# Kernel optimization log

Hardware: AMD Instinct MI355X
Metric: run time of the kernel (lower is better)

The kernel has to match this reference:

```python
import jax, jax.numpy as jnp
import numpy as np
import math
from jax import lax

DIM = 128
D_STATE = 16
D_CONV = 4
EXPAND = 2
NSLICES = 16
D_INNER = EXPAND * DIM          # 256
DT_RANK = math.ceil(DIM / 16)   # 8
B_, H_, W_ = 4, 64, 64
L = H_ * W_                     # 4096


def silu(x):
    return x * jax.nn.sigmoid(x)


def causal_conv1d(x, w, b):
    # x: (b, d, l), w: (d, k) depthwise, b: (d,)  -- causal, output length l
    l = x.shape[-1]
    xp = jnp.pad(x, ((0, 0), (0, 0), (D_CONV - 1, 0)))
    y = sum(w[None, :, k, None] * xp[:, :, k:k + l] for k in range(D_CONV))
    return y + b[None, :, None]


def selective_scan(u, delta, A, B, C):
    # u, delta: (b, d, l); A: (d, n); B, C: (b, n, l)
    bsz, d, l = u.shape
    n = A.shape[1]
    u_t = u.transpose(2, 0, 1)      # (l, b, d)
    d_t = delta.transpose(2, 0, 1)  # (l, b, d)
    B_t = B.transpose(2, 0, 1)      # (l, b, n)
    C_t = C.transpose(2, 0, 1)      # (l, b, n)

    def step(h, inp):
        u_, de_, b_, c_ = inp
        dA = jnp.exp(de_[..., None] * A)                    # (b, d, n)
        h = h * dA + (de_ * u_)[..., None] * b_[:, None, :]  # (b, d, n)
        y = jnp.einsum('bdn,bn->bd', h, c_)
        return h, y

    h0 = jnp.zeros((bsz, d, n), u.dtype)
    _, ys = lax.scan(step, h0, (u_t, d_t, B_t, C_t))
    return ys.transpose(1, 2, 0)  # (b, d, l)


def mamba_dir(xz, conv_w, conv_b, x_proj_w, dt_w, dt_b, A_log, Dp):
    # one directional Mamba branch (conv + S6 scan + silu(z) gating), returns (b, d_inner, l)
    x, z = jnp.split(xz, 2, axis=1)
    x = silu(causal_conv1d(x, conv_w, conv_b))
    x_dbl = jnp.einsum('rd,bdl->brl', x_proj_w, x)          # (b, dt_rank+2n, l)
    dt_raw = x_dbl[:, :DT_RANK]
    Bm = x_dbl[:, DT_RANK:DT_RANK + D_STATE]
    Cm = x_dbl[:, DT_RANK + D_STATE:]
    delta = jax.nn.softplus(jnp.einsum('dr,brl->bdl', dt_w, dt_raw) + dt_b[None, :, None])
    A = -jnp.exp(A_log)
    y = selective_scan(x, delta, A, Bm, Cm)
    y = y + Dp[None, :, None] * x
    return y * silu(z)


def setup_inputs() -> dict:
    key = jax.random.key(0)
    ks = iter(jax.random.split(key, 40))

    def rn(shape, scale=0.02):
        return jax.random.normal(next(ks), shape, dtype=jnp.float32) * scale

    inp = {"x_in": jax.random.normal(next(ks), (B_, H_, W_, DIM), dtype=jnp.float32)}
    inp["in_proj_w"] = rn((2 * D_INNER, DIM))
    for suf in ["", "_b", "_s"]:
        inp["conv_w" + suf] = rn((D_INNER, D_CONV), 0.1)
        inp["conv_b" + suf] = rn((D_INNER,), 0.1)
        inp["x_proj_w" + suf] = rn((DT_RANK + 2 * D_STATE, D_INNER))
        inp["dt_proj_w" + suf] = rn((D_INNER, DT_RANK), 0.1)
        inp["dt_proj_b" + suf] = rn((D_INNER,), 0.1)
        inp["A_log" + suf] = jnp.log(jnp.tile(jnp.arange(1, D_STATE + 1, dtype=jnp.float32), (D_INNER, 1)))
        inp["D" + suf] = jnp.ones((D_INNER,), jnp.float32)
    inp["out_proj_w"] = rn((DIM, D_INNER))
    return inp


def reference(x_in, in_proj_w, conv_w, conv_b, x_proj_w, dt_proj_w, dt_proj_b, A_log, D,
              conv_w_b, conv_b_b, x_proj_w_b, dt_proj_w_b, dt_proj_b_b, A_log_b, D_b,
              conv_w_s, conv_b_s, x_proj_w_s, dt_proj_w_s, dt_proj_b_s, A_log_s, D_s,
              out_proj_w):
    b, h, w, c = x_in.shape
    l = h * w
    x = x_in.reshape(b, l, c)
    xz = jnp.einsum('pd,bld->bpl', in_proj_w, x)  # (b, 2*d_inner, l)

    # forward scan
    y_f = mamba_dir(xz, conv_w, conv_b, x_proj_w, dt_proj_w, dt_proj_b, A_log, D)
    # backward scan (flip along length)
    y_b = jnp.flip(mamba_dir(jnp.flip(xz, -1), conv_w_b, conv_b_b, x_proj_w_b,
                             dt_proj_w_b, dt_proj_b_b, A_log_b, D_b), -1)
    # interleaved-slice scan: chunk length into NSLICES pieces, stack, flatten
    m = l // NSLICES
    xz_s = xz.reshape(b, 2 * D_INNER, NSLICES, m).swapaxes(-1, -2).reshape(b, 2 * D_INNER, l)
    y_s = mamba_dir(xz_s, conv_w_s, conv_b_s, x_proj_w_s, dt_proj_w_s, dt_proj_b_s, A_log_s, D_s)
    y_s = y_s.reshape(b, D_INNER, m, NSLICES).swapaxes(-1, -2).reshape(b, D_INNER, l)

    y = y_f + y_b + y_s
    out = jnp.einsum('od,bdl->blo', out_proj_w, y)
    return out.reshape(b, h, w, c)
```

## Files before the change

### kernel.cpp

```cpp
#include <hip/hip_runtime.h>
#include <math.h>

#define LSEQ 4096

#define XZ_OFF   0ULL
#define XZ_SZ    (4ULL * 4096 * 512)
#define U_OFF    (XZ_OFF + XZ_SZ)
#define DIR_SZ   (4ULL * 256 * 4096)
#define DELTA_OFF (U_OFF + 3ULL * DIR_SZ)
#define BC_OFF   (DELTA_OFF + 3ULL * DIR_SZ)
#define BC_SZ    (4ULL * 4096 * 32)
#define WTIN_OFF DELTA_OFF
#define WTOUT_OFF U_OFF

__device__ __forceinline__ float sigmoidf_(float x) { return 1.0f / (1.0f + __expf(-x)); }
__device__ __forceinline__ float siluf_(float x)    { return x * sigmoidf_(x); }

__device__ __forceinline__ float fast_exp2_asm(float x) {
    float r;
    asm volatile("v_exp_f32 %0, %1\n\ts_nop 0" : "=v"(r) : "v"(x));
    return r;
}
#if defined(__has_builtin)
#if __has_builtin(__builtin_amdgcn_exp2f)
#define EXP2(x) __builtin_amdgcn_exp2f(x)
#else
#define EXP2(x) fast_exp2_asm(x)
#endif
#else
#define EXP2(x) fast_exp2_asm(x)
#endif

__device__ __forceinline__ float softplus_fast(float x) {
    float t = EXP2(1.44269504f * x);
    float r = 0.69314718f * __log2f(1.0f + t);
    return (x > 20.0f) ? x : r;
}

__device__ __forceinline__ int perm_idx(int dir, int j) {
    if (dir == 0) return j;
    if (dir == 1) return 4095 - j;
    return ((j & 15) << 8) | (j >> 4);
}

#define DPP_MOV(x, ctrl) __int_as_float(__builtin_amdgcn_update_dpp(0, __float_as_int(x), (ctrl), 0xF, 0xF, true))

__global__ __launch_bounds__(256) void transpose_in_kernel(const float* __restrict__ w,
                                                           float* __restrict__ wT) {
    int idx = blockIdx.x * 256 + threadIdx.x;
    int p = idx >> 7, c = idx & 127;
    wT[(size_t)c * 512 + p] = w[(size_t)p * 128 + c];
}

__global__ __launch_bounds__(256) void inproj_kernel(const float* __restrict__ x,
                              const float* __restrict__ wT,
                              float* __restrict__ xz) {
    const int b = blockIdx.y;
    const int l0 = blockIdx.x * 16;
    __shared__ float xs[128 * 20];
    for (int idx = threadIdx.x; idx < 16 * 128; idx += 256) {
        int li = idx >> 7, c = idx & 127;
        xs[c * 20 + li] = x[((size_t)(b * 4096 + l0 + li)) * 128 + c];
    }
    __syncthreads();
    const int p0 = (threadIdx.x & 127) * 4;
    const int g8 = (threadIdx.x >> 7) * 8;
    float acc[4][8];
    #pragma unroll
    for (int j = 0; j < 4; ++j)
        #pragma unroll
        for (int k = 0; k < 8; ++k) acc[j][k] = 0.0f;
    for (int c = 0; c < 128; ++c) {
        float4 wv = *(const float4*)(wT + (size_t)c * 512 + p0);
        const float* xp = xs + c * 20 + g8;
        float4 x0 = *(const float4*)(xp);
        float4 x1 = *(const float4*)(xp + 4);
        float xv[8] = {x0.x, x0.y, x0.z, x0.w, x1.x, x1.y, x1.z, x1.w};
        float wj[4] = {wv.x, wv.y, wv.z, wv.w};
        #pragma unroll
        for (int j = 0; j < 4; ++j)
            #pragma unroll
            for (int k = 0; k < 8; ++k) acc[j][k] += wj[j] * xv[k];
    }
    #pragma unroll
    for (int k = 0; k < 8; ++k) {
        float4 s; s.x = acc[0][k]; s.y = acc[1][k]; s.z = acc[2][k]; s.w = acc[3][k];
        *(float4*)(xz + ((size_t)(b * 4096 + l0 + g8 + k)) * 512 + p0) = s;
    }
}

__global__ __launch_bounds__(256) void front_kernel(float* __restrict__ ws,
        const float* __restrict__ xw0, const float* __restrict__ xw1, const float* __restrict__ xw2,
        const float* __restrict__ dw0, const float* __restrict__ dw1, const float* __restrict__ dw2,
        const float* __restrict__ db0, const float* __restrict__ db1, const float* __restrict__ db2,
        const float* __restrict__ cw0, const float* __restrict__ cb0,
        const float* __restrict__ cw1, const float* __restrict__ cb1,
        const float* __restrict__ cw2, const float* __restrict__ cb2) {
    const int l0 = blockIdx.x * 32, b = blockIdx.y, dir = blockIdx.z;
    const float* xw = (dir == 0) ? xw0 : (dir == 1) ? xw1 : xw2;
    const float* dw = (dir == 0) ? dw0 : (dir == 1) ? dw1 : dw2;
    const float* db = (dir == 0) ? db0 : (dir == 1) ? db1 : db2;
    const float* cw = (dir == 0) ? cw0 : (dir == 1) ? cw1 : cw2;
    const float* cb = (dir == 0) ? cb0 : (dir == 1) ? cb1 : cb2;
    const float* xzb = ws + XZ_OFF + (size_t)b * 4096 * 512;
    float* ub      = ws + U_OFF + (size_t)dir * DIR_SZ + (size_t)b * 256 * 4096;
    float* deltab  = ws + DELTA_OFF + (size_t)dir * DIR_SZ + (size_t)b * 256 * 4096;
    float* Bf      = ws + BC_OFF + (size_t)dir * BC_SZ;
    float* Cf      = Bf + BC_SZ / 2;

    __shared__ float xt[35 * 260];
    __shared__ float xd[40 * 33];
    float* ut = xt;

    for (int idx = threadIdx.x; idx < 35 * 64; idx += 256) {
        int k = idx >> 6, dq = idx & 63;
        int j = l0 - 3 + k;
        float4 v = {0.f, 0.f, 0.f, 0.f};
        if (j >= 0) {
            int row = (dir == 0) ? j : (dir == 1) ? (4095 - j) : (((j & 15) << 8) | (j >> 4));
            v = *(const float4*)(xzb + (size_t)row * 512 + dq * 4);
        }
        *(float4*)(xt + k * 260 + dq * 4) = v;
    }
    __syncthreads();

    const int d = threadIdx.x;
    const float w0 = cw[d * 4 + 0], w1 = cw[d * 4 + 1], w2 = cw[d * 4 + 2], w3 = cw[d * 4 + 3];
    const float bb = cb[d];
    float win[35];
    #pragma unroll
    for (int k = 0; k < 35; ++k) win[k] = xt[k * 260 + d];
    float r[32];
    #pragma unroll
    for (int li = 0; li < 32; ++li)
        r[li] = siluf_(bb + w0 * win[li] + w1 * win[li + 1] + w2 * win[li + 2] + w3 * win[li + 3]);
    {
        float* urow = ub + (size_t)d * 4096 + l0;
        #pragma unroll
        for (int q = 0; q < 8; ++q) {
            float4 v; v.x = r[q*4]; v.y = r[q*4+1]; v.z = r[q*4+2]; v.w = r[q*4+3];
            *(float4*)(urow + q * 4) = v;
        }
    }
    __syncthreads();

    #pragma unroll
    for (int li = 0; li < 32; ++li)
        ut[li * 264 + 4 * (((d >> 2) ^ (li & 7))) + (d & 3)] = r[li];
    __syncthreads();

    {
        const int rg = threadIdx.x >> 5;
        const int li = threadIdx.x & 31;
        float acc[5];
        #pragma unroll
        for (int j = 0; j < 5; ++j) acc[j] = 0.0f;
        const float* up = ut + li * 264;
        const int sw = (li & 7);
        #pragma unroll 2
        for (int c4 = 0; c4 < 64; ++c4) {
            float4 uv = *(const float4*)(up + 4 * (c4 ^ sw));
            const int c = 4 * (c4 ^ sw);
            #pragma unroll
            for (int j = 0; j < 5; ++j) {
                float4 wv = *(const float4*)(xw + (size_t)(rg * 5 + j) * 256 + c);
                acc[j] += wv.x * uv.x + wv.y * uv.y + wv.z * uv.z + wv.w * uv.w;
            }
        }
        #pragma unroll
        for (int j = 0; j < 5; ++j) xd[(rg * 5 + j) * 33 + li] = acc[j];
    }
    __syncthreads();

    {
        const int wv = threadIdx.x >> 6;
        const int lane = threadIdx.x & 63;
        const int n = lane >> 2, lq = lane & 3;
        #pragma unroll
        for (int j = 0; j < 2; ++j) {
            int l4 = (l0 >> 2) + j * 4 + wv;
            int li = (j * 4 + wv) * 4 + lq;
            size_t base = (((size_t)b * 1024 + l4) * 16 + n) * 4 + lq;
            Bf[base] = xd[(8 + n) * 33 + li];
            Cf[base] = xd[(24 + n) * 33 + li];
        }
    }
    {
        const int li = threadIdx.x & 31;
        float xr8[8];
        #pragma unroll
        for (int rr = 0; rr < 8; ++rr) xr8[rr] = xd[rr * 33 + li];
        #pragma unroll
        for (int k = 0; k < 32; ++k) {
            int dd = ((threadIdx.x + k * 256) >> 5);
            float4 wa = *(const float4*)(dw + dd * 8);
            float4 wb = *(const float4*)(dw + dd * 8 + 4);
            float acc = db[dd]
                + wa.x * xr8[0] + wa.y * xr8[1] + wa.z * xr8[2] + wa.w * xr8[3]
                + wb.x * xr8[4] + wb.y * xr8[5] + wb.z * xr8[6] + wb.w * xr8[7];
            deltab[(size_t)dd * 4096 + l0 + li] = softplus_fast(acc);
        }
    }
}

__global__ __launch_bounds__(512) void scan_kernel(float* __restrict__ ws,
                            const float* __restrict__ Al0, const float* __restrict__ Dp0,
                            const float* __restrict__ Al1, const float* __restrict__ Dp1,
                            const float* __restrict__ Al2, const float* __restrict__ Dp2) {
    const int d = blockIdx.x, b = blockIdx.y, dir = blockIdx.z;
    const float* Al = (dir == 0) ? Al0 : (dir == 1) ? Al1 : Al2;
    const float* Dp = (dir == 0) ? Dp0 : (dir == 1) ? Dp1 : Dp2;
    const int c = threadIdx.x >> 4;
    const int n = threadIdx.x & 15;
    const int qid = n >> 2;
    const float Ane = -1.44269504f * __expf(Al[d * 16 + n]);
    const float Dd = Dp[d];
    const float* urow = ws + U_OFF + (size_t)dir * DIR_SZ + ((size_t)(b * 256 + d)) * 4096;
    float* drow = ws + DELTA_OFF + (size_t)dir * DIR_SZ + ((size_t)(b * 256 + d)) * 4096;

    __shared__ float sdu[32 * 260];
    __shared__ float red[32 * 34];
    float* Psh = red;
    float* Ssh = red + 512;

    {
        const float4* d4 = (const float4*)drow;
        const float4* u4 = (const float4*)urow;
        for (int i = threadIdx.x; i < 1024; i += 512) {
            float4 dv = d4[i], uv = u4[i];
            int l = i * 4;
            float* p = sdu + (l >> 7) * 260 + (l & 127) * 2;
            float4 a, bq;
            a.x = dv.x; a.y = dv.x * uv.x; a.z = dv.y; a.w = dv.y * uv.y;
            bq.x = dv.z; bq.y = dv.z * uv.z; bq.z = dv.w; bq.w = dv.w * uv.w;
            *(float4*)(p) = a; *(float4*)(p + 4) = bq;
        }
    }
    __syncthreads();

    const float4* Bq = (const float4*)(ws + BC_OFF + (size_t)dir * BC_SZ)
                       + ((size_t)b * 1024 + c * 32) * 16 + n;
    const float4* Cq = (const float4*)(ws + BC_OFF + (size_t)dir * BC_SZ + BC_SZ / 2)
                       + ((size_t)b * 1024 + c * 32) * 16 + n;
    const float4* sp = (const float4*)(sdu + c * 260);

    float S = 0.0f, dsum = 0.0f;
    #pragma unroll 8
    for (int k4 = 0; k4 < 32; ++k4) {
        float4 a = sp[k4 * 2], bq = sp[k4 * 2 + 1];
        float4 Bv = Bq[(size_t)k4 * 16];
        float e0 = EXP2(Ane * a.x), e1 = EXP2(Ane * a.z);
        float e2 = EXP2(Ane * bq.x), e3 = EXP2(Ane * bq.z);
        dsum += (a.x + a.z) + (bq.x + bq.z);
        S = S * e0 + a.y * Bv.x;
        S = S * e1 + a.w * Bv.y;
        S = S * e2 + bq.y * Bv.z;
        S = S * e3 + bq.w * Bv.w;
    }
    Ssh[c * 16 + n] = S;
    Psh[c * 16 + n] = EXP2(Ane * dsum);
    __syncthreads();
    float h = 0.0f;
    for (int k = 0; k < c; ++k) h = h * Psh[k * 16 + n] + Ssh[k * 16 + n];
    __syncthreads();

    #define SCAN_STEP(t, ee, du, Bn, Cn) { \
        h = h * (ee) + (du) * (Bn); \
        float yp = h * (Cn); \
        yp += DPP_MOV(yp, 0xB1); \
        yp += DPP_MOV(yp, 0x4E); \
        red[(4 * (t) + qid) * 34 + c] = yp; }

    for (int g = 0; g < 16; ++g) {
        float4 a0 = sp[g * 4 + 0], a1 = sp[g * 4 + 1];
        float4 a2 = sp[g * 4 + 2], a3 = sp[g * 4 + 3];
        float4 Bv0 = Bq[(size_t)(g * 2) * 16], Bv1 = Bq[(size_t)(g * 2 + 1) * 16];
        float4 Cv0 = Cq[(size_t)(g * 2) * 16], Cv1 = Cq[(size_t)(g * 2 + 1) * 16];
        float e0 = EXP2(Ane * a0.x), e1 = EXP2(Ane * a0.z);
        float e2 = EXP2(Ane * a1.x), e3 = EXP2(Ane * a1.z);
        float e4 = EXP2(Ane * a2.x), e5 = EXP2(Ane * a2.z);
        float e6 = EXP2(Ane * a3.x), e7 = EXP2(Ane * a3.z);
        SCAN_STEP(0, e0, a0.y, Bv0.x, Cv0.x)
        SCAN_STEP(1, e1, a0.w, Bv0.y, Cv0.y)
        SCAN_STEP(2, e2, a1.y, Bv0.z, Cv0.z)
        SCAN_STEP(3, e3, a1.w, Bv0.w, Cv0.w)
        SCAN_STEP(4, e4, a2.y, Bv1.x, Cv1.x)
        SCAN_STEP(5, e5, a2.w, Bv1.y, Cv1.y)
        SCAN_STEP(6, e6, a3.y, Bv1.z, Cv1.z)
        SCAN_STEP(7, e7, a3.w, Bv1.w, Cv1.w)
        const int tt = n & 7;
        float q0 = red[(4 * tt + 0) * 34 + c];
        float q1 = red[(4 * tt + 1) * 34 + c];
        float q2 = red[(4 * tt + 2) * 34 + c];
        float q3 = red[(4 * tt + 3) * 34 + c];
        float y = (q0 + q1) + (q2 + q3);
        if (n < 8) {
            int gl = c * 128 + g * 8 + n;
            drow[perm_idx(dir, gl)] = y + Dd * urow[gl];
        }
    }
    #undef SCAN_STEP
}

__global__ __launch_bounds__(256) void transpose_w_kernel(const float* __restrict__ ow,
                                                          float* __restrict__ wT) {
    int idx = blockIdx.x * 256 + threadIdx.x;
    int o = idx >> 8, d = idx & 255;
    wT[(size_t)d * 128 + o] = ow[(size_t)o * 256 + d];
}

__global__ __launch_bounds__(256) void epilogue_kernel(const float* __restrict__ ws,
                                const float* __restrict__ wT,
                                float* __restrict__ out) {
    const int l0 = blockIdx.x * 16, b = blockIdx.y;
    __shared__ float yt[256 * 20];
    const float* yf = ws + DELTA_OFF;
    const float* yb = ws + DELTA_OFF + DIR_SZ;
    const float* ysd = ws + DELTA_OFF + 2 * DIR_SZ;
    const float* xzb = ws + XZ_OFF + (size_t)b * 4096 * 512;

    for (int idx = threadIdx.x; idx < 256 * 4; idx += 256) {
        int d = idx >> 2, q = (idx & 3) * 4;
        size_t ro = ((size_t)(b * 256 + d)) * 4096 + l0 + q;
        float4 vf = *(const float4*)(yf + ro);
        float4 vb = *(const float4*)(yb + ro);
        float4 vs = *(const float4*)(ysd + ro);
        float4 s; s.x = vf.x + vb.x + vs.x; s.y = vf.y + vb.y + vs.y;
        s.z = vf.z + vb.z + vs.z; s.w = vf.w + vb.w + vs.w;
        *(float4*)(yt + d * 20 + q) = s;
    }
    __syncthreads();
    {
        const int d = threadIdx.x;
        #pragma unroll 4
        for (int li = 0; li < 16; ++li) {
            float z = xzb[(size_t)(l0 + li) * 512 + 256 + d];
            yt[d * 20 + li] *= siluf_(z);
        }
    }
    __syncthreads();

    const int o0 = (threadIdx.x & 31) * 4;
    const int lp = (threadIdx.x >> 5) * 2;
    float a0[4], a1[4];
    #pragma unroll
    for (int j = 0; j < 4; ++j) { a0[j] = 0.0f; a1[j] = 0.0f; }
    #pragma unroll 4
    for (int d = 0; d < 256; ++d) {
        float4 w = *(const float4*)(wT + (size_t)d * 128 + o0);
        float2 y = *(const float2*)(yt + d * 20 + lp);
        a0[0] += w.x * y.x; a0[1] += w.y * y.x; a0[2] += w.z * y.x; a0[3] += w.w * y.x;
        a1[0] += w.x * y.y; a1[1] += w.y * y.y; a1[2] += w.z * y.y; a1[3] += w.w * y.y;
    }
    float4 s0; s0.x = a0[0]; s0.y = a0[1]; s0.z = a0[2]; s0.w = a0[3];
    float4 s1; s1.x = a1[0]; s1.y = a1[1]; s1.z = a1[2]; s1.w = a1[3];
    *(float4*)(out + ((size_t)(b * 4096 + l0 + lp)) * 128 + o0) = s0;
    *(float4*)(out + ((size_t)(b * 4096 + l0 + lp + 1)) * 128 + o0) = s1;
}

extern "C" void kernel_launch(void* const* d_in, const int* in_sizes, int n_in,
                              void* d_out, int out_size, void* d_ws, size_t ws_size,
                              hipStream_t stream) {
    const float* x_in = (const float*)d_in[0];
    const float* ipw  = (const float*)d_in[1];
    const float* cw[3]  = {(const float*)d_in[2],  (const float*)d_in[9],  (const float*)d_in[16]};
    const float* cb[3]  = {(const float*)d_in[3],  (const float*)d_in[10], (const float*)d_in[17]};
    const float* xpw[3] = {(const float*)d_in[4],  (const float*)d_in[11], (const float*)d_in[18]};
    const float* dtw[3] = {(const float*)d_in[5],  (const float*)d_in[12], (const float*)d_in[19]};
    const float* dtb[3] = {(const float*)d_in[6],  (const float*)d_in[13], (const float*)d_in[20]};
    const float* alog[3]= {(const float*)d_in[7],  (const float*)d_in[14], (const float*)d_in[21]};
    const float* dp[3]  = {(const float*)d_in[8],  (const float*)d_in[15], (const float*)d_in[22]};
    const float* ow   = (const float*)d_in[23];
    float* ws  = (float*)d_ws;
    float* out = (float*)d_out;

    transpose_in_kernel<<<dim3(256), 256, 0, stream>>>(ipw, ws + WTIN_OFF);
    inproj_kernel<<<dim3(256, 4), 256, 0, stream>>>(x_in, ws + WTIN_OFF, ws);
    front_kernel<<<dim3(128, 4, 3), 256, 0, stream>>>(ws,
        xpw[0], xpw[1], xpw[2], dtw[0], dtw[1], dtw[2], dtb[0], dtb[1], dtb[2],
        cw[0], cb[0], cw[1], cb[1], cw[2], cb[2]);
    scan_kernel<<<dim3(256, 4, 3), 512, 0, stream>>>(ws,
        alog[0], dp[0], alog[1], dp[1], alog[2], dp[2]);
    transpose_w_kernel<<<dim3(128), 256, 0, stream>>>(ow, ws + WTOUT_OFF);
    epilogue_kernel<<<dim3(256, 4), 256, 0, stream>>>(ws, ws + WTOUT_OFF, out);
}
```

Before: 419.0 us.

## Stage projection weights in LDS tiles and pack scan math into vector ops

The x_proj stage and the out_proj epilogue now copy weight tiles cooperatively into shared memory in chunks, instead of every thread reading weights straight from global memory. The scan kernel changes the sdu layout to separate delta and delta*u float4s. It also uses 2-wide vector multiplies and explicit FMAs, and folds delta*u*B into one product before the recurrence. The aim is to cut redundant global or L2 weight traffic and ALU instruction count, at the cost of extra LDS usage and more barriers, which may reduce occupancy.

Result: faster. 379.0 us (-9.6%).

```diff
diff --git a/kernel.cpp b/kernel.cpp
--- a/kernel.cpp
+++ b/kernel.cpp
@@ -12,6 +12,9 @@
 #define BC_SZ    (4ULL * 4096 * 32)
 #define WTIN_OFF DELTA_OFF
 #define WTOUT_OFF U_OFF
+
+typedef float v2f __attribute__((ext_vector_type(2)));
+typedef float v4f __attribute__((ext_vector_type(4)));
 
 __device__ __forceinline__ float sigmoidf_(float x) { return 1.0f / (1.0f + __expf(-x)); }
 __device__ __forceinline__ float siluf_(float x)    { return x * sigmoidf_(x); }
@@ -110,6 +113,7 @@
 
     __shared__ float xt[35 * 260];
     __shared__ float xd[40 * 33];
+    __shared__ float xws[40 * 68];
     float* ut = xt;
 
     for (int idx = threadIdx.x; idx < 35 * 64; idx += 256) {
@@ -147,7 +151,6 @@
     #pragma unroll
     for (int li = 0; li < 32; ++li)
         ut[li * 264 + 4 * (((d >> 2) ^ (li & 7))) + (d & 3)] = r[li];
-    __syncthreads();
 
     {
         const int rg = threadIdx.x >> 5;
@@ -157,14 +160,22 @@
         for (int j = 0; j < 5; ++j) acc[j] = 0.0f;
         const float* up = ut + li * 264;
         const int sw = (li & 7);
-        #pragma unroll 2
-        for (int c4 = 0; c4 < 64; ++c4) {
-            float4 uv = *(const float4*)(up + 4 * (c4 ^ sw));
-            const int c = 4 * (c4 ^ sw);
-            #pragma unroll
-            for (int j = 0; j < 5; ++j) {
-                float4 wv = *(const float4*)(xw + (size_t)(rg * 5 + j) * 256 + c);
-                acc[j] += wv.x * uv.x + wv.y * uv.y + wv.z * uv.z + wv.w * uv.w;
+        for (int ct = 0; ct < 4; ++ct) {
+            __syncthreads();
+            for (int idx = threadIdx.x; idx < 40 * 16; idx += 256) {
+                int rr = idx >> 4, q = (idx & 15) * 4;
+                *(float4*)(xws + rr * 68 + q) = *(const float4*)(xw + (size_t)rr * 256 + ct * 64 + q);
+            }
+            __syncthreads();
+            #pragma unroll 4
+            for (int c4t = 0; c4t < 16; ++c4t) {
+                const int cc = 4 * (c4t ^ sw);
+                float4 uv = *(const float4*)(up + ct * 64 + cc);
+                #pragma unroll
+                for (int j = 0; j < 5; ++j) {
+                    float4 wv = *(const float4*)(xws + (rg * 5 + j) * 68 + cc);
+                    acc[j] += wv.x * uv.x + wv.y * uv.y + wv.z * uv.z + wv.w * uv.w;
+                }
             }
         }
         #pragma unroll
@@ -214,6 +225,7 @@
     const int n = threadIdx.x & 15;
     const int qid = n >> 2;
     const float Ane = -1.44269504f * __expf(Al[d * 16 + n]);
+    const v2f AneD = {Ane, Ane};
     const float Dd = Dp[d];
     const float* urow = ws + U_OFF + (size_t)dir * DIR_SZ + ((size_t)(b * 256 + d)) * 4096;
     float* drow = ws + DELTA_OFF + (size_t)dir * DIR_SZ + ((size_t)(b * 256 + d)) * 4096;
@@ -230,64 +242,70 @@
             float4 dv = d4[i], uv = u4[i];
             int l = i * 4;
             float* p = sdu + (l >> 7) * 260 + (l & 127) * 2;
-            float4 a, bq;
-            a.x = dv.x; a.y = dv.x * uv.x; a.z = dv.y; a.w = dv.y * uv.y;
-            bq.x = dv.z; bq.y = dv.z * uv.z; bq.z = dv.w; bq.w = dv.w * uv.w;
-            *(float4*)(p) = a; *(float4*)(p + 4) = bq;
-        }
-    }
-    __syncthreads();
-
-    const float4* Bq = (const float4*)(ws + BC_OFF + (size_t)dir * BC_SZ)
+            float4 du;
+            du.x = dv.x * uv.x; du.y = dv.y * uv.y; du.z = dv.z * uv.z; du.w = dv.w * uv.w;
+            *(float4*)(p) = dv; *(float4*)(p + 4) = du;
+        }
+    }
+    __syncthreads();
+
+    const v4f* Bq = (const v4f*)(ws + BC_OFF + (size_t)dir * BC_SZ)
                        + ((size_t)b * 1024 + c * 32) * 16 + n;
-    const float4* Cq = (const float4*)(ws + BC_OFF + (size_t)dir * BC_SZ + BC_SZ / 2)
+    const v4f* Cq = (const v4f*)(ws + BC_OFF + (size_t)dir * BC_SZ + BC_SZ / 2)
                        + ((size_t)b * 1024 + c * 32) * 16 + n;
-    const float4* sp = (const float4*)(sdu + c * 260);
-
-    float S = 0.0f, dsum = 0.0f;
+    const v4f* sp = (const v4f*)(sdu + c * 260);
+
+    float S = 0.0f;
+    v2f ds2 = {0.0f, 0.0f};
     #pragma unroll 8
     for (int k4 = 0; k4 < 32; ++k4) {
-        float4 a = sp[k4 * 2], bq = sp[k4 * 2 + 1];
-        float4 Bv = Bq[(size_t)k4 * 16];
-        float e0 = EXP2(Ane * a.x), e1 = EXP2(Ane * a.z);
-        float e2 = EXP2(Ane * bq.x), e3 = EXP2(Ane * bq.z);
-        dsum += (a.x + a.z) + (bq.x + bq.z);
-        S = S * e0 + a.y * Bv.x;
-        S = S * e1 + a.w * Bv.y;
-        S = S * e2 + bq.y * Bv.z;
-        S = S * e3 + bq.w * Bv.w;
+        v4f dq = sp[k4 * 2], uq = sp[k4 * 2 + 1];
+        v4f Bv = Bq[(size_t)k4 * 16];
+        v2f t0 = AneD * dq.xy;
+        v2f t1 = AneD * dq.zw;
+        v2f p0 = uq.xy * Bv.xy;
+        v2f p1 = uq.zw * Bv.zw;
+        ds2 += dq.xy + dq.zw;
+        S = __builtin_fmaf(S, EXP2(t0.x), p0.x);
+        S = __builtin_fmaf(S, EXP2(t0.y), p0.y);
+        S = __builtin_fmaf(S, EXP2(t1.x), p1.x);
+        S = __builtin_fmaf(S, EXP2(t1.y), p1.y);
     }
     Ssh[c * 16 + n] = S;
-    Psh[c * 16 + n] = EXP2(Ane * dsum);
+    Psh[c * 16 + n] = EXP2(Ane * (ds2.x + ds2.y));
     __syncthreads();
     float h = 0.0f;
     for (int k = 0; k < c; ++k) h = h * Psh[k * 16 + n] + Ssh[k * 16 + n];
     __syncthreads();
 
-    #define SCAN_STEP(t, ee, du, Bn, Cn) { \
-        h = h * (ee) + (du) * (Bn); \
+    #define SCAN_STEP(t, ee, pp, Cn) { \
+        h = __builtin_fmaf(h, (ee), (pp)); \
         float yp = h * (Cn); \
         yp += DPP_MOV(yp, 0xB1); \
         yp += DPP_MOV(yp, 0x4E); \
         red[(4 * (t) + qid) * 34 + c] = yp; }
 
     for (int g = 0; g < 16; ++g) {
-        float4 a0 = sp[g * 4 + 0], a1 = sp[g * 4 + 1];
-        float4 a2 = sp[g * 4 + 2], a3 = sp[g * 4 + 3];
-        float4 Bv0 = Bq[(size_t)(g * 2) * 16], Bv1 = Bq[(size_t)(g * 2 + 1) * 16];
-        float4 Cv0 = Cq[(size_t)(g * 2) * 16], Cv1 = Cq[(size_t)(g * 2 + 1) * 16];
-        float e0 = EXP2(Ane * a0.x), e1 = EXP2(Ane * a0.z);
-        float e2 = EXP2(Ane * a1.x), e3 = EXP2(Ane * a1.z);
-        float e4 = EXP2(Ane * a2.x), e5 = EXP2(Ane * a2.z);
-        float e6 = EXP2(Ane * a3.x), e7 = EXP2(Ane * a3.z);
-        SCAN_STEP(0, e0, a0.y, Bv0.x, Cv0.x)
-        SCAN_STEP(1, e1, a0.w, Bv0.y, Cv0.y)
-        SCAN_STEP(2, e2, a1.y, Bv0.z, Cv0.z)
-        SCAN_STEP(3, e3, a1.w, Bv0.w, Cv0.w)
-        SCAN_STEP(4, e4, a2.y, Bv1.x, Cv1.x)
-        SCAN_STEP(5, e5, a2.w, Bv1.y, Cv1.y)
-        SCAN_STEP(6, e6, a3.y, Bv1.z, Cv1.z)
-        SCAN_STEP(7, e7, a3.w, Bv1.w, Cv1.w)
+        v4f d0 = sp[g * 4 + 0], u0 = sp[g * 4 + 1];
+        v4f d1 = sp[g * 4 + 2], u1 = sp[g * 4 + 3];
+        v4f Bv0 = Bq[(size_t)(g * 2) * 16], Bv1 = Bq[(size_t)(g * 2 + 1) * 16];
+        v4f Cv0 = Cq[(size_t)(g * 2) * 16], Cv1 = Cq[(size_t)(g * 2 + 1) * 16];
+        v2f t0 = AneD * d0.xy, t1 = AneD * d0.zw;
+        v2f t2 = AneD * d1.xy, t3 = AneD * d1.zw;
+        v2f p0 = u0.xy * Bv0.xy, p1 = u0.zw * Bv0.zw;
+        v2f p2 = u1.xy * Bv1.xy, p3 = u1.zw * Bv1.zw;
+        float e0 = EXP2(t0.x), e1 = EXP2(t0.y);
+        float e2 = EXP2(t1.x), e3 = EXP2(t1.y);
+        float e4 = EXP2(t2.x), e5 = EXP2(t2.y);
+        float e6 = EXP2(t3.x), e7 = EXP2(t3.y);
+        SCAN_STEP(0, e0, p0.x, Cv0.x)
+        SCAN_STEP(1, e1, p0.y, Cv0.y)
+        SCAN_STEP(2, e2, p1.x, Cv0.z)
+        SCAN_STEP(3, e3, p1.y, Cv0.w)
+        SCAN_STEP(4, e4, p2.x, Cv1.x)
+        SCAN_STEP(5, e5, p2.y, Cv1.y)
+        SCAN_STEP(6, e6, p3.x, Cv1.z)
+        SCAN_STEP(7, e7, p3.y, Cv1.w)
         const int tt = n & 7;
         float q0 = red[(4 * tt + 0) * 34 + c];
         float q1 = red[(4 * tt + 1) * 34 + c];
@@ -314,6 +332,7 @@
                                 float* __restrict__ out) {
     const int l0 = blockIdx.x * 16, b = blockIdx.y;
     __shared__ float yt[256 * 20];
+    __shared__ float wts[64 * 128];
     const float* yf = ws + DELTA_OFF;
     const float* yb = ws + DELTA_OFF + DIR_SZ;
     const float* ysd = ws + DELTA_OFF + 2 * DIR_SZ;
@@ -338,19 +357,26 @@
             yt[d * 20 + li] *= siluf_(z);
         }
     }
-    __syncthreads();
 
     const int o0 = (threadIdx.x & 31) * 4;
     const int lp = (threadIdx.x >> 5) * 2;
     float a0[4], a1[4];
     #pragma unroll
     for (int j = 0; j < 4; ++j) { a0[j] = 0.0f; a1[j] = 0.0f; }
-    #pragma unroll 4
-    for (int d = 0; d < 256; ++d) {
-        float4 w = *(const float4*)(wT + (size_t)d * 128 + o0);
-        float2 y = *(const float2*)(yt + d * 20 + lp);
-        a0[0] += w.x * y.x; a0[1] += w.y * y.x; a0[2] += w.z * y.x; a0[3] += w.w * y.x;
-        a1[0] += w.x * y.y; a1[1] += w.y * y.y; a1[2] += w.z * y.y; a1[3] += w.w * y.y;
+    for (int dt = 0; dt < 4; ++dt) {
+        __syncthreads();
+        for (int idx = threadIdx.x; idx < 64 * 32; idx += 256) {
+            int dd = idx >> 5, q = (idx & 31) * 4;
+            *(float4*)(wts + dd * 128 + q) = *(const float4*)(wT + (size_t)(dt * 64 + dd) * 128 + q);
+        }
+        __syncthreads();
+        #pragma unroll 4
+        for (int dl = 0; dl < 64; ++dl) {
+            float4 w = *(const float4*)(wts + dl * 128 + o0);
+            float2 y = *(const float2*)(yt + (dt * 64 + dl) * 20 + lp);
+            a0[0] += w.x * y.x; a0[1] += w.y * y.x; a0[2] += w.z * y.x; a0[3] += w.w * y.x;
+            a1[0] += w.x * y.y; a1[1] += w.y * y.y; a1[2] += w.z * y.y; a1[3] += w.w * y.y;
+        }
     }
     float4 s0; s0.x = a0[0]; s0.y = a0[1]; s0.z = a0[2]; s0.w = a0[3];
     float4 s1; s1.x = a1[0]; s1.y = a1[1]; s1.z = a1[2]; s1.w = a1[3];
```
